# Kernel optimization log

Hardware: AMD Instinct MI355X
Metric: run time of the kernel (lower is better)

## Reference

```python
import jax, jax.numpy as jnp
import numpy as np

B_SZ, L, D_MODEL, D_STATE = 8, 2048, 1024, 64
LN_EPS = 1e-5


def setup_inputs() -> dict:
    key = jax.random.key(0)
    ks = jax.random.split(key, 12)
    x = jax.random.normal(ks[0], (B_SZ, L, D_MODEL), dtype=jnp.float32)
    # input projection (nn.Linear)
    W_in = jax.random.normal(ks[1], (D_MODEL, D_MODEL), dtype=jnp.float32) / np.sqrt(D_MODEL)
    b_in = jnp.zeros((D_MODEL,), dtype=jnp.float32)
    # LayerNorm affine
    gamma = jnp.ones((D_MODEL,), dtype=jnp.float32)
    beta = jnp.zeros((D_MODEL,), dtype=jnp.float32)
    # SSM params as real/imag pairs (torch stores cfloat); init per _init_state_space
    A_re = -jax.random.uniform(ks[2], (D_STATE,), dtype=jnp.float32) * 0.1
    A_im = jax.random.normal(ks[3], (D_STATE,), dtype=jnp.float32) * 0.1
    B_re = jax.random.normal(ks[4], (D_STATE,), dtype=jnp.float32) * 0.0004
    B_im = jax.random.normal(ks[5], (D_STATE,), dtype=jnp.float32) * 0.0004
    C_re = jax.random.normal(ks[6], (D_MODEL, D_STATE), dtype=jnp.float32) * 0.0004
    C_im = jax.random.normal(ks[7], (D_MODEL, D_STATE), dtype=jnp.float32) * 0.0004
    D_re = jax.random.normal(ks[8], (D_MODEL,), dtype=jnp.float32) * 0.02
    D_im = jax.random.normal(ks[9], (D_MODEL,), dtype=jnp.float32) * 0.02
    return {"x": x, "W_in": W_in, "b_in": b_in, "gamma": gamma, "beta": beta,
            "A_re": A_re, "A_im": A_im, "B_re": B_re, "B_im": B_im,
            "C_re": C_re, "C_im": C_im, "D_re": D_re, "D_im": D_im}


def _forward(x, W_in, b_in, gamma, beta, A_re, A_im, B_re, B_im, C_re, C_im, D_re, D_im):
    # input projection + LayerNorm
    x = jnp.einsum('bld,de->ble', x, W_in.T) + b_in
    mu = jnp.mean(x, axis=-1, keepdims=True)
    var = jnp.mean(jnp.square(x - mu), axis=-1, keepdims=True)
    x = (x - mu) * jax.lax.rsqrt(var + LN_EPS) * gamma + beta

    Lc = x.shape[1]
    A = A_re + 1j * A_im          # (N,)
    Bp = B_re + 1j * B_im         # (N,)
    Cp = C_re + 1j * C_im         # (M, N)
    Dp = D_re + 1j * D_im         # (M,)
    # A^l via exp(l * log A) -> (L, N), stable for autodiff
    pows = jnp.exp(jnp.arange(Lc, dtype=jnp.float32)[:, None] * jnp.log(A)[None, :])
    # fused kernel generation: K[l, m] = sum_n A^l[n] * B[n] * C[m, n]  (+ D broadcast on all taps, per source)
    K = jnp.einsum('ln,n,mn->lm', pows, Bp, Cp) + Dp[None, :]  # (L, M) complex

    # causal depthwise long convolution via FFT: y[t, m] = sum_{s<=t} K[s, m] * x[t-s, m]
    n = 2 * Lc
    Xf = jnp.fft.fft(x.astype(jnp.complex64), n=n, axis=1)   # (B, 2L, M)
    Kf = jnp.fft.fft(K, n=n, axis=0)                          # (2L, M)
    y = jnp.fft.ifft(Xf * Kf[None], axis=1)[:, :Lc, :].real   # real part (standard S4 convention)

    return y.astype(x.dtype) + x  # dropout=0 (eval); residual


def reference(x, W_in, b_in, gamma, beta, A_re, A_im, B_re, B_im, C_re, C_im, D_re, D_im):
    return _forward(x, W_in, b_in, gamma, beta, A_re, A_im, B_re, B_im, C_re, C_im, D_re, D_im)
```

## Files before the change

### kernel.cpp

```cpp
#include <hip/hip_runtime.h>
#include <stdint.h>


typedef __attribute__((ext_vector_type(8))) short short8;
typedef __attribute__((ext_vector_type(8))) unsigned short ushort8;
typedef __attribute__((ext_vector_type(4))) unsigned short ushort4v;
typedef __attribute__((ext_vector_type(4))) float f32x4;
typedef unsigned short ushort;

#define L_SEQ 2048
#define DM    1024
#define TT    8
#define NC    16
#define CL    128

__device__ __forceinline__ ushort f2bf(float f) {
  uint32_t u = __builtin_bit_cast(uint32_t, f);
  u += 0x7FFFu + ((u >> 16) & 1u);
  return (ushort)(u >> 16);
}
__device__ __forceinline__ float bf2f(ushort u) {
  uint32_t w = ((uint32_t)u) << 16;
  return __builtin_bit_cast(float, w);
}
__device__ __forceinline__ void gload16(const void* g, void* lds_p) {
  __builtin_amdgcn_global_load_lds(
      (const __attribute__((address_space(1))) uint32_t*)g,
      (__attribute__((address_space(3))) uint32_t*)lds_p, 16, 0, 0);
}

__global__ __launch_bounds__(256) void cvt_x(const float* __restrict__ x,
                                             ushort* __restrict__ Xbf) {
  int g = blockIdx.x * 256 + threadIdx.x;
  const f32x4* src = (const f32x4*)x;
  f32x4 v[8];
  #pragma unroll
  for (int k = 0; k < 8; ++k)
    v[k] = __builtin_nontemporal_load(&src[(size_t)g + (size_t)k * 524288]);
  #pragma unroll
  for (int k = 0; k < 8; ++k) {
    ushort4v o;
    #pragma unroll
    for (int e = 0; e < 4; ++e) o[e] = f2bf(v[k][e]);
    *(ushort4v*)(Xbf + ((size_t)g + (size_t)k * 524288) * 4) = o;
  }
}

__global__ __launch_bounds__(256) void wcvt_kgen(
    const float* __restrict__ W, ushort* __restrict__ Wbf,
    const float* __restrict__ A_re, const float* __restrict__ A_im,
    const float* __restrict__ B_re, const float* __restrict__ B_im,
    const float* __restrict__ C_re, const float* __restrict__ C_im,
    float* __restrict__ Khat) {
  int blk = blockIdx.x;
  int tid = threadIdx.x;
  if (blk < 128) {
    int g = blk * 256 + tid;
    #pragma unroll
    for (int k = 0; k < 4; ++k) {
      int i = g + k * 32768;
      const f32x4* s = (const f32x4*)W + (size_t)i * 2;
      f32x4 a = s[0], b = s[1];
      ushort8 o;
      #pragma unroll
      for (int e = 0; e < 4; ++e) { o[e] = f2bf(a[e]); o[4 + e] = f2bf(b[e]); }
      *(ushort8*)(Wbf + (size_t)i * 8) = o;
    }
    return;
  }
  int s = (blk - 128) >> 2;
  int m = ((blk - 128) & 3) * 256 + tid;
  __shared__ float Pr[64], Pi[64];
  if (tid < 64) {
    float ar = A_re[tid], ai = A_im[tid];
    float pr = 1.f, pi = 0.f;
    for (int k = 0; k < s; ++k) { float n = pr * ar - pi * ai; pi = pr * ai + pi * ar; pr = n; }
    float br = B_re[tid], bi = B_im[tid];
    Pr[tid] = pr * br - pi * bi;
    Pi[tid] = pr * bi + pi * br;
  }
  __syncthreads();
  const float* cr = C_re + (size_t)m * 64;
  const float* ci = C_im + (size_t)m * 64;
  float acc = 0.f;
  #pragma unroll
  for (int n = 0; n < 64; ++n) acc += Pr[n] * cr[n] - Pi[n] * ci[n];
  Khat[(size_t)s * DM + m] = acc;
}

#define SBAR() do { asm volatile("" ::: "memory"); __builtin_amdgcn_s_barrier(); asm volatile("" ::: "memory"); } while (0)
#define LGKM0() asm volatile("s_waitcnt lgkmcnt(0)" ::: "memory")

#define RD_A(ABASE, MH)                                                            \
  { _Pragma("unroll") for (int mi_ = 0; mi_ < 4; ++mi_) {                          \
      int row_ = wr * 128 + (MH) * 64 + mi_ * 16 + fr;                             \
      const char* rp_ = (const char*)(ABASE) + row_ * 128;                         \
      _Pragma("unroll") for (int kk_ = 0; kk_ < 2; ++kk_) {                        \
        int slot_ = kk_ * 4 + kg;                                                  \
        areg[mi_][kk_] = *(const short8*)(rp_ + (((slot_ ^ (row_ & 7)) << 4)));    \
      } } }

#define RD_B(DST, BBASE, NH)                                                       \
  { _Pragma("unroll") for (int ni_ = 0; ni_ < 2; ++ni_) {                          \
      int row_ = wn * 64 + (NH) * 32 + ni_ * 16 + fr;                              \
      const char* rp_ = (const char*)(BBASE) + row_ * 128;                         \
      _Pragma("unroll") for (int kk_ = 0; kk_ < 2; ++kk_) {                        \
        int slot_ = kk_ * 4 + kg;                                                  \
        DST[ni_][kk_] = *(const short8*)(rp_ + (((slot_ ^ (row_ & 7)) << 4)));     \
      } } }

#define MF(MH, NH, BV)                                                             \
  { _Pragma("unroll") for (int mi_ = 0; mi_ < 4; ++mi_)                            \
      _Pragma("unroll") for (int ni_ = 0; ni_ < 2; ++ni_) {                        \
        acc[(MH)*4+mi_][(NH)*2+ni_] = __builtin_amdgcn_mfma_f32_16x16x32_bf16(     \
            areg[mi_][0], BV[ni_][0], acc[(MH)*4+mi_][(NH)*2+ni_], 0, 0, 0);       \
        acc[(MH)*4+mi_][(NH)*2+ni_] = __builtin_amdgcn_mfma_f32_16x16x32_bf16(     \
            areg[mi_][1], BV[ni_][1], acc[(MH)*4+mi_][(NH)*2+ni_], 0, 0, 0); } }

#define STAGE(LDSHALF, GROW, TTI)                                                  \
  { const ushort* g_ = (GROW) + (size_t)(wid * 16 + rl) * DM + (TTI) * 64 + sl * 8;\
    gload16(g_,          (LDSHALF) + wid * 1024);                                  \
    gload16(g_ + 8 * DM, (LDSHALF) + wid * 1024 + 512); }

__global__ __launch_bounds__(512, 2) void gemm_bias(const ushort* __restrict__ Xb,
                                                    const ushort* __restrict__ Wb,
                                                    const float* __restrict__ bias,
                                                    ushort* __restrict__ Yb,
                                                    float2* __restrict__ rowpart) {
  extern __shared__ ushort lds[];
  ushort* A0 = lds;
  ushort* B0 = lds + 16384;
  ushort* A1 = lds + 32768;
  ushort* B1 = lds + 49152;

  int wg = blockIdx.x;
  int swz = (wg & 7) * 32 + (wg >> 3);
  int bm = swz >> 2, bn = swz & 3;
  int tid = threadIdx.x;
  int lane = tid & 63, wid = tid >> 6;
  int wr = wid >> 2, wn = wid & 3;
  int fr = lane & 15, kg = lane >> 4;
  int rl = lane >> 3, sl = (lane & 7) ^ rl;

  const ushort* XgT = Xb + (size_t)(bm * 256) * DM;
  const ushort* XgB = XgT + (size_t)128 * DM;
  const ushort* WgT = Wb + (size_t)(bn * 256) * DM;
  const ushort* WgX = WgT + (size_t)128 * DM;

  f32x4 acc[8][4];
  #pragma unroll
  for (int i = 0; i < 8; ++i)
    #pragma unroll
    for (int j = 0; j < 4; ++j) acc[i][j] = (f32x4){0.f, 0.f, 0.f, 0.f};
  short8 areg[4][2], bt[2][2], bb[2][2];

  STAGE(A0,         XgT, 0);
  STAGE(A0 + 8192,  XgB, 0);
  STAGE(B0,         WgT, 0);
  STAGE(B0 + 8192,  WgX, 0);
  STAGE(B1,         WgT, 1);
  STAGE(B1 + 8192,  WgX, 1);
  asm volatile("s_waitcnt vmcnt(4)" ::: "memory");
  SBAR();

  #pragma unroll 1
  for (int t = 0; t < 8; ++t) {
    int o = 2 * t + 1, n0 = 2 * t + 2, n1 = 2 * t + 3;
    bool stg = (t < 7);
    RD_A(A0, 0); RD_B(bt, B0, 0);
    STAGE(A1, XgT, o);
    SBAR(); LGKM0();
    __builtin_amdgcn_s_setprio(1); MF(0, 0, bt); __builtin_amdgcn_s_setprio(0);
    SBAR();
    RD_B(bb, B0, 1);
    STAGE(A1 + 8192, XgB, o);
    SBAR(); LGKM0();
    __builtin_amdgcn_s_setprio(1); MF(0, 1, bb); __builtin_amdgcn_s_setprio(0);
    SBAR();
    RD_A(A0, 1);
    if (stg) STAGE(B0, WgT, n0);
    SBAR(); LGKM0();
    __builtin_amdgcn_s_setprio(1); MF(1, 1, bb); __builtin_amdgcn_s_setprio(0);
    SBAR();
    if (stg) {
      STAGE(B0 + 8192, WgX, n0);
      asm volatile("s_waitcnt vmcnt(4)" ::: "memory");
    } else {
      asm volatile("s_waitcnt vmcnt(0)" ::: "memory");
    }
    SBAR(); LGKM0();
    __builtin_amdgcn_s_setprio(1); MF(1, 0, bt); __builtin_amdgcn_s_setprio(0);
    SBAR();
    RD_A(A1, 0); RD_B(bt, B1, 0);
    if (stg) STAGE(A0, XgT, n0);
    SBAR(); LGKM0();
    __builtin_amdgcn_s_setprio(1); MF(0, 0, bt); __builtin_amdgcn_s_setprio(0);
    SBAR();
    RD_B(bb, B1, 1);
    if (stg) STAGE(A0 + 8192, XgB, n0);
    SBAR(); LGKM0();
    __builtin_amdgcn_s_setprio(1); MF(0, 1, bb); __builtin_amdgcn_s_setprio(0);
    SBAR();
    RD_A(A1, 1);
    if (stg) STAGE(B1, WgT, n1);
    SBAR(); LGKM0();
    __builtin_amdgcn_s_setprio(1); MF(1, 1, bb); __builtin_amdgcn_s_setprio(0);
    SBAR();
    if (stg) {
      STAGE(B1 + 8192, WgX, n1);
      asm volatile("s_waitcnt vmcnt(4)" ::: "memory");
    } else {
      asm volatile("s_waitcnt vmcnt(0)" ::: "memory");
    }
    SBAR(); LGKM0();
    __builtin_amdgcn_s_setprio(1); MF(1, 0, bt); __builtin_amdgcn_s_setprio(0);
    SBAR();
  }

  asm volatile("s_waitcnt vmcnt(0) lgkmcnt(0)" ::: "memory");
  __syncthreads();
  float* lsS = (float*)lds;
  float* lsQ = lsS + 1024;
  int fq = lane >> 4;
  float bv[4];
  #pragma unroll
  for (int ni = 0; ni < 4; ++ni) bv[ni] = bias[bn * 256 + wn * 64 + ni * 16 + fr];
  #pragma unroll
  for (int mi = 0; mi < 8; ++mi) {
    float rs_[4] = {0.f, 0.f, 0.f, 0.f}, rq_[4] = {0.f, 0.f, 0.f, 0.f};
    #pragma unroll
    for (int ni = 0; ni < 4; ++ni) {
      int gcol = bn * 256 + wn * 64 + ni * 16 + fr;
      #pragma unroll
      for (int j = 0; j < 4; ++j) {
        float v = acc[mi][ni][j] + bv[ni];
        int grow = bm * 256 + wr * 128 + mi * 16 + fq * 4 + j;
        Yb[(size_t)grow * DM + gcol] = f2bf(v);
        rs_[j] += v; rq_[j] += v * v;
      }
    }
    #pragma unroll
    for (int d = 1; d < 16; d <<= 1)
      #pragma unroll
      for (int j = 0; j < 4; ++j) {
        rs_[j] += __shfl_xor(rs_[j], d);
        rq_[j] += __shfl_xor(rq_[j], d);
      }
    if (fr == 0) {
      #pragma unroll
      for (int j = 0; j < 4; ++j) {
        int r = wr * 128 + mi * 16 + fq * 4 + j;
        lsS[wn * 256 + r] = rs_[j];
        lsQ[wn * 256 + r] = rq_[j];
      }
    }
  }
  __syncthreads();
  if (tid < 256) {
    float s = lsS[tid] + lsS[256 + tid] + lsS[512 + tid] + lsS[768 + tid];
    float q = lsQ[tid] + lsQ[256 + tid] + lsQ[512 + tid] + lsQ[768 + tid];
    rowpart[((size_t)(bm * 256 + tid)) * 4 + bn] = make_float2(s, q);
  }
}

__device__ __forceinline__ void row_stats(const float2* __restrict__ rowpart,
                                          int grow, float& mu_, float& rs_) {
  float s = 0.f, q = 0.f;
  #pragma unroll
  for (int n = 0; n < 4; ++n) { float2 p = rowpart[(size_t)grow * 4 + n]; s += p.x; q += p.y; }
  mu_ = s * (1.f / DM);
  float v = q * (1.f / DM) - mu_ * mu_;
  rs_ = rsqrtf(v + 1e-5f);
}

__global__ __launch_bounds__(256) void chunksum(const ushort* __restrict__ ybf,
                                                const float2* __restrict__ rowpart,
                                                const float* __restrict__ gamma,
                                                const float* __restrict__ beta,
                                                float* __restrict__ partial) {
  int blk = blockIdx.x;
  int b = blk >> 5, c = (blk >> 1) & 15, mg = blk & 1;
  int tid = threadIdx.x;
  int m2 = mg * 512 + tid * 2;
  int bb = b * L_SEQ, cs = c * CL;
  __shared__ float muL[CL], rsL[CL];
  if (tid < CL) row_stats(rowpart, bb + cs + tid, muL[tid], rsL[tid]);
  __syncthreads();
  float g0 = gamma[m2], g1 = gamma[m2 + 1], be0 = beta[m2], be1 = beta[m2 + 1];
  float s0 = 0.f, s1 = 0.f;
  const ushort* base = ybf + (size_t)(bb + cs) * DM + m2;
  #pragma unroll 8
  for (int t = 0; t < CL; ++t) {
    uint32_t v = *(const uint32_t*)(base + (size_t)t * DM);
    float f0 = bf2f((ushort)v), f1 = bf2f((ushort)(v >> 16));
    float r = rsL[t], mu_ = muL[t];
    s0 += (f0 - mu_) * r * g0 + be0;
    s1 += (f1 - mu_) * r * g1 + be1;
  }
  *(float2*)&partial[((size_t)(b * NC + c)) * DM + m2] = make_float2(s0, s1);
}

__global__ __launch_bounds__(256) void ssm2(const ushort* __restrict__ ybf,
                                            const float2* __restrict__ rowpart,
                                            const float* __restrict__ gamma,
                                            const float* __restrict__ beta,
                                            const float* __restrict__ Khat,
                                            const float* __restrict__ D_re,
                                            const float* __restrict__ partial,
                                            float* __restrict__ Out) {
  int blk = blockIdx.x;
  int b = blk >> 6, c = (blk >> 2) & 15, mg = blk & 3;
  int tid = threadIdx.x;
  int m = mg * 256 + tid;
  int bb = b * L_SEQ, cs = c * CL;

  __shared__ float muL[CL + TT], rsL[CL + TT];
  for (int r = tid; r < CL + TT; r += 256) {
    int row = cs - TT + r;
    if (row >= 0) row_stats(rowpart, bb + row, muL[r], rsL[r]);
    else { muL[r] = 0.f; rsL[r] = 0.f; }
  }
  __syncthreads();

  float kh[TT];
  #pragma unroll
  for (int s = 0; s < TT; ++s) kh[s] = Khat[(size_t)s * DM + m];
  float g = gamma[m], be = beta[m], dre = D_re[m];

  float run = 0.f;
  for (int cc = 0; cc < c; ++cc) run += partial[((size_t)(b * NC + cc)) * DM + m];

  float P[TT], A[32];
  if (c == 0) {
    #pragma unroll
    for (int i = 0; i < TT; ++i) P[i] = 0.f;
  } else {
    #pragma unroll
    for (int i = 0; i < TT; ++i) {
      float v = bf2f(ybf[(size_t)(bb + cs - TT + i) * DM + m]);
      P[i] = (v - muL[i]) * rsL[i] * g + be;
    }
  }
  #pragma unroll
  for (int i = 0; i < 32; ++i) {
    float v = bf2f(ybf[(size_t)(bb + cs + i) * DM + m]);
    A[i] = (v - muL[TT + i]) * rsL[TT + i] * g + be;
  }

  #pragma unroll 1
  for (int j = 0; j < CL / 32; ++j) {
    float B[32];
    if (j < CL / 32 - 1) {
      int tb = (j + 1) * 32;
      #pragma unroll
      for (int i = 0; i < 32; ++i) {
        float v = bf2f(ybf[(size_t)(bb + cs + tb + i) * DM + m]);
        B[i] = (v - muL[TT + tb + i]) * rsL[TT + tb + i] * g + be;
      }
    }
    #pragma unroll
    for (int i = 0; i < 32; ++i) {
      float fir = 0.f;
      #pragma unroll
      for (int s = 0; s < TT; ++s) {
        float xv = (i - s >= 0) ? A[i - s] : P[TT + i - s];
        fir += kh[s] * xv;
      }
      run += A[i];
      Out[(size_t)(bb + cs + j * 32 + i) * DM + m] = A[i] + fir + dre * run;
    }
    #pragma unroll
    for (int i = 0; i < TT; ++i) P[i] = A[32 - TT + i];
    #pragma unroll
    for (int i = 0; i < 32; ++i) A[i] = B[i];
  }
}

extern "C" void kernel_launch(void* const* d_in, const int* in_sizes, int n_in,
                              void* d_out, int out_size, void* d_ws, size_t ws_size,
                              hipStream_t stream) {
  const float* x     = (const float*)d_in[0];
  const float* W     = (const float*)d_in[1];
  const float* b_in  = (const float*)d_in[2];
  const float* gamma = (const float*)d_in[3];
  const float* beta  = (const float*)d_in[4];
  const float* A_re  = (const float*)d_in[5];
  const float* A_im  = (const float*)d_in[6];
  const float* B_re  = (const float*)d_in[7];
  const float* B_im  = (const float*)d_in[8];
  const float* C_re  = (const float*)d_in[9];
  const float* C_im  = (const float*)d_in[10];
  const float* D_re  = (const float*)d_in[11];

  char* ws = (char*)d_ws;
  ushort* Wbf     = (ushort*)(ws + 0);
  ushort* ybf     = (ushort*)(ws + 2097152);
  float2* rowpart = (float2*)(ws + 35651584);
  float*  partial = (float*)(ws + 36175872);
  float*  khat    = (float*)(ws + 36700160);

  ushort* Xbf = (ushort*)d_out;
  float*  out = (float*)d_out;

  (void)hipFuncSetAttribute((const void*)gemm_bias,
                            hipFuncAttributeMaxDynamicSharedMemorySize, 131072);

  wcvt_kgen<<<160, 256, 0, stream>>>(W, Wbf, A_re, A_im, B_re, B_im, C_re, C_im, khat);
  cvt_x<<<2048, 256, 0, stream>>>(x, Xbf);
  gemm_bias<<<256, 512, 131072, stream>>>(Xbf, Wbf, b_in, ybf, rowpart);
  chunksum<<<256, 256, 0, stream>>>(ybf, rowpart, gamma, beta, partial);
  ssm2<<<512, 256, 0, stream>>>(ybf, rowpart, gamma, beta, khat, D_re, partial, out);
}
```

Measured before the change: 97.63 us.

## Fuse fp32-to-bf16 conversion of x into GEMM A-operand load path

Removes the separate cvt_x kernel and has the GEMM stage fp32 x tiles directly into LDS, converting to bf16 with v_cvt_pk_bf16_f32 while reading A fragments. Because fp32 A tiles take twice the LDS, the M tile is halved from 256 to 128 rows and the grid doubles to 512 blocks, with the tile swizzle and epilogue row-stat reduction adjusted to match. This saves one full read and write pass over x and a kernel launch. In exchange it raises global traffic for A, adds conversion ALU work in the inner loop, and lowers the per-block arithmetic intensity.

```diff
diff --git a/kernel.cpp b/kernel.cpp
--- a/kernel.cpp
+++ b/kernel.cpp
@@ -4,8 +4,8 @@
 
 typedef __attribute__((ext_vector_type(8))) short short8;
 typedef __attribute__((ext_vector_type(8))) unsigned short ushort8;
-typedef __attribute__((ext_vector_type(4))) unsigned short ushort4v;
 typedef __attribute__((ext_vector_type(4))) float f32x4;
+typedef __attribute__((ext_vector_type(4))) uint32_t uint32x4;
 typedef unsigned short ushort;
 
 #define L_SEQ 2048
@@ -27,23 +27,6 @@
   __builtin_amdgcn_global_load_lds(
       (const __attribute__((address_space(1))) uint32_t*)g,
       (__attribute__((address_space(3))) uint32_t*)lds_p, 16, 0, 0);
-}
-
-__global__ __launch_bounds__(256) void cvt_x(const float* __restrict__ x,
-                                             ushort* __restrict__ Xbf) {
-  int g = blockIdx.x * 256 + threadIdx.x;
-  const f32x4* src = (const f32x4*)x;
-  f32x4 v[8];
-  #pragma unroll
-  for (int k = 0; k < 8; ++k)
-    v[k] = __builtin_nontemporal_load(&src[(size_t)g + (size_t)k * 524288]);
-  #pragma unroll
-  for (int k = 0; k < 8; ++k) {
-    ushort4v o;
-    #pragma unroll
-    for (int e = 0; e < 4; ++e) o[e] = f2bf(v[k][e]);
-    *(ushort4v*)(Xbf + ((size_t)g + (size_t)k * 524288) * 4) = o;
-  }
 }
 
 __global__ __launch_bounds__(256) void wcvt_kgen(
@@ -90,15 +73,21 @@
 
 #define SBAR() do { asm volatile("" ::: "memory"); __builtin_amdgcn_s_barrier(); asm volatile("" ::: "memory"); } while (0)
 #define LGKM0() asm volatile("s_waitcnt lgkmcnt(0)" ::: "memory")
-
-#define RD_A(ABASE, MH)                                                            \
-  { _Pragma("unroll") for (int mi_ = 0; mi_ < 4; ++mi_) {                          \
-      int row_ = wr * 128 + (MH) * 64 + mi_ * 16 + fr;                             \
-      const char* rp_ = (const char*)(ABASE) + row_ * 128;                         \
+#define CVTPK(D, S0, S1) asm("v_cvt_pk_bf16_f32 %0, %1, %2" : "=v"(D) : "v"(S0), "v"(S1))
+
+#define RD_A(ABASE_F, MH)                                                          \
+  { _Pragma("unroll") for (int mi_ = 0; mi_ < 2; ++mi_) {                          \
+      int row_ = wr * 64 + (MH) * 32 + mi_ * 16 + fr;                              \
+      const char* rp_ = (const char*)(ABASE_F) + row_ * 256;                       \
       _Pragma("unroll") for (int kk_ = 0; kk_ < 2; ++kk_) {                        \
-        int slot_ = kk_ * 4 + kg;                                                  \
-        areg[mi_][kk_] = *(const short8*)(rp_ + (((slot_ ^ (row_ & 7)) << 4)));    \
-      } } }
+        int s0_ = kk_ * 8 + kg * 2;                                                \
+        f32x4 lo_ = *(const f32x4*)(rp_ + ((s0_ ^ fr) << 4));                      \
+        f32x4 hi_ = *(const f32x4*)(rp_ + (((s0_ + 1) ^ fr) << 4));                \
+        uint32_t u0_, u1_, u2_, u3_;                                               \
+        CVTPK(u0_, lo_[0], lo_[1]); CVTPK(u1_, lo_[2], lo_[3]);                    \
+        CVTPK(u2_, hi_[0], hi_[1]); CVTPK(u3_, hi_[2], hi_[3]);                    \
+        uint32x4 uu_ = {u0_, u1_, u2_, u3_};                                       \
+        areg[mi_][kk_] = __builtin_bit_cast(short8, uu_); } } }
 
 #define RD_B(DST, BBASE, NH)                                                       \
   { _Pragma("unroll") for (int ni_ = 0; ni_ < 2; ++ni_) {                          \
@@ -110,31 +99,38 @@
       } } }
 
 #define MF(MH, NH, BV)                                                             \
-  { _Pragma("unroll") for (int mi_ = 0; mi_ < 4; ++mi_)                            \
+  { _Pragma("unroll") for (int mi_ = 0; mi_ < 2; ++mi_)                            \
       _Pragma("unroll") for (int ni_ = 0; ni_ < 2; ++ni_) {                        \
-        acc[(MH)*4+mi_][(NH)*2+ni_] = __builtin_amdgcn_mfma_f32_16x16x32_bf16(     \
-            areg[mi_][0], BV[ni_][0], acc[(MH)*4+mi_][(NH)*2+ni_], 0, 0, 0);       \
-        acc[(MH)*4+mi_][(NH)*2+ni_] = __builtin_amdgcn_mfma_f32_16x16x32_bf16(     \
-            areg[mi_][1], BV[ni_][1], acc[(MH)*4+mi_][(NH)*2+ni_], 0, 0, 0); } }
-
-#define STAGE(LDSHALF, GROW, TTI)                                                  \
+        acc[(MH)*2+mi_][(NH)*2+ni_] = __builtin_amdgcn_mfma_f32_16x16x32_bf16(     \
+            areg[mi_][0], BV[ni_][0], acc[(MH)*2+mi_][(NH)*2+ni_], 0, 0, 0);       \
+        acc[(MH)*2+mi_][(NH)*2+ni_] = __builtin_amdgcn_mfma_f32_16x16x32_bf16(     \
+            areg[mi_][1], BV[ni_][1], acc[(MH)*2+mi_][(NH)*2+ni_], 0, 0, 0); } }
+
+#define STAGE_A(AHALF_F, GROW, TTI)                                                \
+  { _Pragma("unroll") for (int j_ = 0; j_ < 2; ++j_) {                             \
+      int row_ = wid * 8 + j_ * 4 + (lane >> 4);                                   \
+      int gs_ = (lane & 15) ^ (row_ & 15);                                         \
+      const float* g_ = (GROW) + (size_t)row_ * DM + (TTI) * 64 + gs_ * 4;         \
+      gload16(g_, (AHALF_F) + (wid * 8 + j_ * 4) * 64); } }
+
+#define STAGE_B(LDSHALF, GROW, TTI)                                                \
   { const ushort* g_ = (GROW) + (size_t)(wid * 16 + rl) * DM + (TTI) * 64 + sl * 8;\
     gload16(g_,          (LDSHALF) + wid * 1024);                                  \
     gload16(g_ + 8 * DM, (LDSHALF) + wid * 1024 + 512); }
 
-__global__ __launch_bounds__(512, 2) void gemm_bias(const ushort* __restrict__ Xb,
+__global__ __launch_bounds__(512, 2) void gemm_bias(const float* __restrict__ X,
                                                     const ushort* __restrict__ Wb,
                                                     const float* __restrict__ bias,
                                                     ushort* __restrict__ Yb,
                                                     float2* __restrict__ rowpart) {
   extern __shared__ ushort lds[];
-  ushort* A0 = lds;
-  ushort* B0 = lds + 16384;
-  ushort* A1 = lds + 32768;
-  ushort* B1 = lds + 49152;
+  float*  A0f = (float*)lds;
+  float*  A1f = A0f + 8192;
+  ushort* B0  = lds + 32768;
+  ushort* B1  = lds + 49152;
 
   int wg = blockIdx.x;
-  int swz = (wg & 7) * 32 + (wg >> 3);
+  int swz = (wg & 7) * 64 + (wg >> 3);
   int bm = swz >> 2, bn = swz & 3;
   int tid = threadIdx.x;
   int lane = tid & 63, wid = tid >> 6;
@@ -142,24 +138,24 @@
   int fr = lane & 15, kg = lane >> 4;
   int rl = lane >> 3, sl = (lane & 7) ^ rl;
 
-  const ushort* XgT = Xb + (size_t)(bm * 256) * DM;
-  const ushort* XgB = XgT + (size_t)128 * DM;
+  const float* XgT = X + (size_t)(bm * 128) * DM;
+  const float* XgB = XgT + (size_t)64 * DM;
   const ushort* WgT = Wb + (size_t)(bn * 256) * DM;
   const ushort* WgX = WgT + (size_t)128 * DM;
 
-  f32x4 acc[8][4];
-  #pragma unroll
-  for (int i = 0; i < 8; ++i)
+  f32x4 acc[4][4];
+  #pragma unroll
+  for (int i = 0; i < 4; ++i)
     #pragma unroll
     for (int j = 0; j < 4; ++j) acc[i][j] = (f32x4){0.f, 0.f, 0.f, 0.f};
-  short8 areg[4][2], bt[2][2], bb[2][2];
-
-  STAGE(A0,         XgT, 0);
-  STAGE(A0 + 8192,  XgB, 0);
-  STAGE(B0,         WgT, 0);
-  STAGE(B0 + 8192,  WgX, 0);
-  STAGE(B1,         WgT, 1);
-  STAGE(B1 + 8192,  WgX, 1);
+  short8 areg[2][2], bt[2][2], bb[2][2];
+
+  STAGE_A(A0f,        XgT, 0);
+  STAGE_A(A0f + 4096, XgB, 0);
+  STAGE_B(B0,         WgT, 0);
+  STAGE_B(B0 + 8192,  WgX, 0);
+  STAGE_B(B1,         WgT, 1);
+  STAGE_B(B1 + 8192,  WgX, 1);
   asm volatile("s_waitcnt vmcnt(4)" ::: "memory");
   SBAR();
 
@@ -167,23 +163,23 @@
   for (int t = 0; t < 8; ++t) {
     int o = 2 * t + 1, n0 = 2 * t + 2, n1 = 2 * t + 3;
     bool stg = (t < 7);
-    RD_A(A0, 0); RD_B(bt, B0, 0);
-    STAGE(A1, XgT, o);
+    RD_A(A0f, 0); RD_B(bt, B0, 0);
+    STAGE_A(A1f, XgT, o);
     SBAR(); LGKM0();
     __builtin_amdgcn_s_setprio(1); MF(0, 0, bt); __builtin_amdgcn_s_setprio(0);
     SBAR();
     RD_B(bb, B0, 1);
-    STAGE(A1 + 8192, XgB, o);
+    STAGE_A(A1f + 4096, XgB, o);
     SBAR(); LGKM0();
     __builtin_amdgcn_s_setprio(1); MF(0, 1, bb); __builtin_amdgcn_s_setprio(0);
     SBAR();
-    RD_A(A0, 1);
-    if (stg) STAGE(B0, WgT, n0);
+    RD_A(A0f, 1);
+    if (stg) STAGE_B(B0, WgT, n0);
     SBAR(); LGKM0();
     __builtin_amdgcn_s_setprio(1); MF(1, 1, bb); __builtin_amdgcn_s_setprio(0);
     SBAR();
     if (stg) {
-      STAGE(B0 + 8192, WgX, n0);
+      STAGE_B(B0 + 8192, WgX, n0);
       asm volatile("s_waitcnt vmcnt(4)" ::: "memory");
     } else {
       asm volatile("s_waitcnt vmcnt(0)" ::: "memory");
@@ -191,23 +187,23 @@
     SBAR(); LGKM0();
     __builtin_amdgcn_s_setprio(1); MF(1, 0, bt); __builtin_amdgcn_s_setprio(0);
     SBAR();
-    RD_A(A1, 0); RD_B(bt, B1, 0);
-    if (stg) STAGE(A0, XgT, n0);
+    RD_A(A1f, 0); RD_B(bt, B1, 0);
+    if (stg) STAGE_A(A0f, XgT, n0);
     SBAR(); LGKM0();
     __builtin_amdgcn_s_setprio(1); MF(0, 0, bt); __builtin_amdgcn_s_setprio(0);
     SBAR();
     RD_B(bb, B1, 1);
-    if (stg) STAGE(A0 + 8192, XgB, n0);
+    if (stg) STAGE_A(A0f + 4096, XgB, n0);
     SBAR(); LGKM0();
     __builtin_amdgcn_s_setprio(1); MF(0, 1, bb); __builtin_amdgcn_s_setprio(0);
     SBAR();
-    RD_A(A1, 1);
-    if (stg) STAGE(B1, WgT, n1);
+    RD_A(A1f, 1);
+    if (stg) STAGE_B(B1, WgT, n1);
     SBAR(); LGKM0();
     __builtin_amdgcn_s_setprio(1); MF(1, 1, bb); __builtin_amdgcn_s_setprio(0);
     SBAR();
     if (stg) {
-      STAGE(B1 + 8192, WgX, n1);
+      STAGE_B(B1 + 8192, WgX, n1);
       asm volatile("s_waitcnt vmcnt(4)" ::: "memory");
     } else {
       asm volatile("s_waitcnt vmcnt(0)" ::: "memory");
@@ -220,13 +216,13 @@
   asm volatile("s_waitcnt vmcnt(0) lgkmcnt(0)" ::: "memory");
   __syncthreads();
   float* lsS = (float*)lds;
-  float* lsQ = lsS + 1024;
+  float* lsQ = lsS + 512;
   int fq = lane >> 4;
   float bv[4];
   #pragma unroll
   for (int ni = 0; ni < 4; ++ni) bv[ni] = bias[bn * 256 + wn * 64 + ni * 16 + fr];
   #pragma unroll
-  for (int mi = 0; mi < 8; ++mi) {
+  for (int mi = 0; mi < 4; ++mi) {
     float rs_[4] = {0.f, 0.f, 0.f, 0.f}, rq_[4] = {0.f, 0.f, 0.f, 0.f};
     #pragma unroll
     for (int ni = 0; ni < 4; ++ni) {
@@ -234,7 +230,7 @@
       #pragma unroll
       for (int j = 0; j < 4; ++j) {
         float v = acc[mi][ni][j] + bv[ni];
-        int grow = bm * 256 + wr * 128 + mi * 16 + fq * 4 + j;
+        int grow = bm * 128 + wr * 64 + mi * 16 + fq * 4 + j;
         Yb[(size_t)grow * DM + gcol] = f2bf(v);
         rs_[j] += v; rq_[j] += v * v;
       }
@@ -249,17 +245,17 @@
     if (fr == 0) {
       #pragma unroll
       for (int j = 0; j < 4; ++j) {
-        int r = wr * 128 + mi * 16 + fq * 4 + j;
-        lsS[wn * 256 + r] = rs_[j];
-        lsQ[wn * 256 + r] = rq_[j];
+        int r = wr * 64 + mi * 16 + fq * 4 + j;
+        lsS[wn * 128 + r] = rs_[j];
+        lsQ[wn * 128 + r] = rq_[j];
       }
     }
   }
   __syncthreads();
-  if (tid < 256) {
-    float s = lsS[tid] + lsS[256 + tid] + lsS[512 + tid] + lsS[768 + tid];
-    float q = lsQ[tid] + lsQ[256 + tid] + lsQ[512 + tid] + lsQ[768 + tid];
-    rowpart[((size_t)(bm * 256 + tid)) * 4 + bn] = make_float2(s, q);
+  if (tid < 128) {
+    float s = lsS[tid] + lsS[128 + tid] + lsS[256 + tid] + lsS[384 + tid];
+    float q = lsQ[tid] + lsQ[128 + tid] + lsQ[256 + tid] + lsQ[384 + tid];
+    rowpart[((size_t)(bm * 128 + tid)) * 4 + bn] = make_float2(s, q);
   }
 }
 
@@ -399,15 +395,13 @@
   float*  partial = (float*)(ws + 36175872);
   float*  khat    = (float*)(ws + 36700160);
 
-  ushort* Xbf = (ushort*)d_out;
-  float*  out = (float*)d_out;
+  float* out = (float*)d_out;
 
   (void)hipFuncSetAttribute((const void*)gemm_bias,
                             hipFuncAttributeMaxDynamicSharedMemorySize, 131072);
 
   wcvt_kgen<<<160, 256, 0, stream>>>(W, Wbf, A_re, A_im, B_re, B_im, C_re, C_im, khat);
-  cvt_x<<<2048, 256, 0, stream>>>(x, Xbf);
-  gemm_bias<<<256, 512, 131072, stream>>>(Xbf, Wbf, b_in, ybf, rowpart);
+  gemm_bias<<<512, 512, 131072, stream>>>(x, Wbf, b_in, ybf, rowpart);
   chunksum<<<256, 256, 0, stream>>>(ybf, rowpart, gamma, beta, partial);
   ssm2<<<512, 256, 0, stream>>>(ybf, rowpart, gamma, beta, khat, D_re, partial, out);
 }
```

Result: faster. 91.76 us (-6.0%).
